# Optimization experiments

Hardware: AMD Instinct MI355X
Metric: run time of the kernel (lower is better)

The kernel has to match this reference:

```python
import jax, jax.numpy as jnp
import numpy as np

B, S, H, NH = 2, 2048, 2048, 16
HD = H // NH


def setup_inputs() -> dict:
    key = jax.random.key(0)
    ks = jax.random.split(key, 10)
    s = 1.0 / np.sqrt(H)
    x = jax.random.normal(ks[0], (B, S, H), dtype=jnp.float32)
    # additive causal mask: 0 on/below diagonal, -1e9 above
    causal = jnp.tril(jnp.ones((S, S), dtype=bool))
    mask = jnp.where(causal, 0.0, -1e9).astype(jnp.float32)[None, None]
    return {
        "x": x,
        "mask": mask,
        "wq": jax.random.normal(ks[1], (H, H), jnp.float32) * s,
        "bq": jnp.zeros((H,), jnp.float32),
        "wk": jax.random.normal(ks[2], (H, H), jnp.float32) * s,
        "bk": jnp.zeros((H,), jnp.float32),
        "wv": jax.random.normal(ks[3], (H, H), jnp.float32) * s,
        "bv": jnp.zeros((H,), jnp.float32),
        "wo": jax.random.normal(ks[4], (H, H), jnp.float32) * s,
        "bo": jnp.zeros((H,), jnp.float32),
    }


def reference(x, mask, wq, bq, wk, bk, wv, bv, wo, bo):
    b, s, _ = x.shape
    scale = HD ** (-0.5)
    # projections -> [b, nh, s, hd]
    def split_heads(t):
        return t.reshape(b, s, NH, HD).transpose(0, 2, 1, 3)
    q = split_heads(x @ wq + bq)
    k = split_heads(x @ wk + bk)
    v = split_heads(x @ wv + bv)
    scores = jnp.einsum('bhqd,bhkd->bhqk', q, k) * scale + mask
    attn = jax.nn.softmax(scores, axis=-1)
    out = jnp.einsum('bhqk,bhkd->bhqd', attn, v)
    out = out.transpose(0, 2, 1, 3).reshape(b, s, H)
    return out @ wo + bo
```

## Files before the change

### kernel.cpp

```cpp
#include <hip/hip_runtime.h>


using bf16x8 = __attribute__((ext_vector_type(8))) short;
using bf16x4 = __attribute__((ext_vector_type(4))) short;
using f32x4  = __attribute__((ext_vector_type(4))) float;

#define S_LEN 2048
#define NHEAD 16
#define HDIM  128
#define HID   2048

__device__ __forceinline__ unsigned short f2bf(float f) {
    unsigned int u = __float_as_uint(f);
    u += 0x7fffu + ((u >> 16) & 1u);
    return (unsigned short)(u >> 16);
}
__device__ __forceinline__ void gl2lds16(const void* g, void* l) {
    __builtin_amdgcn_global_load_lds(
        (const __attribute__((address_space(1))) void*)g,
        (__attribute__((address_space(3))) void*)l, 16, 0, 0);
}

__device__ __forceinline__ f32x4 pv_mfma(bf16x4 a, bf16x4 b, f32x4 c) {
#if defined(__HIP_DEVICE_COMPILE__)
#if __has_builtin(__builtin_amdgcn_mfma_f32_16x16x16bf16_1k)
    return __builtin_amdgcn_mfma_f32_16x16x16bf16_1k(a, b, c, 0, 0, 0);
#else
    asm("v_mfma_f32_16x16x16_bf16 %0, %1, %2, %0" : "+v"(c) : "v"(a), "v"(b));
    return c;
#endif
#else
    (void)a; (void)b;
    return c;
#endif
}

__global__ void convert_all(const float* __restrict__ x,
                            const float* __restrict__ w0, const float* __restrict__ w1,
                            const float* __restrict__ w2, const float* __restrict__ w3,
                            unsigned short* __restrict__ xb,
                            unsigned short* __restrict__ t0, unsigned short* __restrict__ t1,
                            unsigned short* __restrict__ t2, unsigned short* __restrict__ t3) {
    int z = blockIdx.z;
    if (z >= 4) {
        int lin = (z - 4) * 1024 + blockIdx.y * 32 + blockIdx.x;
        int i = (lin * 256 + threadIdx.x) * 4;
        float4 v = *(const float4*)(x + i);
        ushort4 o;
        o.x = f2bf(v.x); o.y = f2bf(v.y); o.z = f2bf(v.z); o.w = f2bf(v.w);
        *(ushort4*)(xb + i) = o;
        return;
    }
    __shared__ float tile[64][65];
    const float* src = (z == 0) ? w0 : (z == 1) ? w1 : (z == 2) ? w2 : w3;
    unsigned short* dst = (z == 0) ? t0 : (z == 1) ? t1 : (z == 2) ? t2 : t3;
    int r0 = blockIdx.y * 64, c0 = blockIdx.x * 64;
    int t = threadIdx.x;
    for (int i = t; i < 64 * 64; i += 256) {
        int r = i >> 6, c = i & 63;
        tile[r][c] = src[(size_t)(r0 + r) * HID + c0 + c];
    }
    __syncthreads();
    for (int i = t; i < 64 * 64; i += 256) {
        int r = i & 63, c = i >> 6;
        dst[(size_t)(c0 + c) * HID + r0 + r] = f2bf(tile[r][c]);
    }
}

__device__ __forceinline__ void sched0() { __builtin_amdgcn_sched_barrier(0); }
__device__ __forceinline__ void w_lgkm8() { asm volatile("s_waitcnt lgkmcnt(8)" ::: "memory"); sched0(); }
__device__ __forceinline__ void w_lgkm4() { asm volatile("s_waitcnt lgkmcnt(4)" ::: "memory"); sched0(); }
__device__ __forceinline__ void w_lgkm0() { asm volatile("s_waitcnt lgkmcnt(0)" ::: "memory"); sched0(); }
__device__ __forceinline__ void w_vm6() { asm volatile("s_waitcnt vmcnt(6)" ::: "memory"); sched0(); }
__device__ __forceinline__ void w_vm4() { asm volatile("s_waitcnt vmcnt(4)" ::: "memory"); sched0(); }
__device__ __forceinline__ void w_vm2() { asm volatile("s_waitcnt vmcnt(2)" ::: "memory"); sched0(); }
__device__ __forceinline__ void w_vm0() { asm volatile("s_waitcnt vmcnt(0)" ::: "memory"); sched0(); }
__device__ __forceinline__ void barx() {
    asm volatile("" ::: "memory");
    __builtin_amdgcn_s_barrier();
    asm volatile("" ::: "memory");
}

__launch_bounds__(512, 2)
__global__ void gemm8p(const unsigned short* __restrict__ A,
                       const unsigned short* __restrict__ Bt,
                       const float* __restrict__ bias0,
                       const float* __restrict__ bias1,
                       const float* __restrict__ bias2,
                       unsigned short* __restrict__ C0,
                       unsigned short* __restrict__ C1,
                       unsigned short* __restrict__ C2) {
    __shared__ __align__(16) unsigned short lds[65536];
    unsigned short* const A0 = lds;
    unsigned short* const A1 = lds + 16384;
    unsigned short* const B0 = lds + 32768;
    unsigned short* const B1 = lds + 49152;

    int vb = (blockIdx.x & 7) * 48 + (blockIdx.x >> 3);
    int m0  = (vb & 15) * 256;
    int n0g = (vb >> 4) * 256;
    int z   = n0g >> 11;
    int nb0 = n0g & 2047;

    int tid = threadIdx.x;
    int lane = tid & 63;
    int wv_ = tid >> 6;
    int wr = wv_ >> 2, wc = wv_ & 3;
    int l15 = lane & 15, quad = lane >> 4;

    int tr = tid >> 3;
    int tc = ((tid & 7) ^ (tr & 7)) << 3;
    const unsigned short* gA = A  + (size_t)(m0  + tr) * HID + tc;
    const unsigned short* gB = Bt + (size_t)(n0g + tr) * HID + tc;
    const int td8 = tid * 8;

    int arow0 = (wr * 128 + l15) * 64;
    int brow0 = (wc * 64 + l15) * 64;
    int swz[2] = { ((quad ^ (l15 & 7)) << 3), (((4 + quad) ^ (l15 & 7)) << 3) };

    f32x4 acc[8][4];
#pragma unroll
    for (int i = 0; i < 8; ++i)
#pragma unroll
        for (int j = 0; j < 4; ++j) acc[i][j] = (f32x4){0.f, 0.f, 0.f, 0.f};

    bf16x8 av[2][4];
    bf16x8 bv[2][2][2];

#define SGA(kt, half, AD) do {                                               \
    size_t _g = (size_t)((half) * 128) * HID + (size_t)(kt) * 64;            \
    gl2lds16(gA + _g,            (AD) + (half) * 8192 + td8);                \
    gl2lds16(gA + _g + 64 * HID, (AD) + (half) * 8192 + 4096 + td8); } while (0)

#define SGB(kt, half, BD) do {                                               \
    size_t _g = (size_t)((half) * 128) * HID + (size_t)(kt) * 64;            \
    gl2lds16(gB + _g,            (BD) + (half) * 8192 + td8);                \
    gl2lds16(gB + _g + 64 * HID, (BD) + (half) * 8192 + 4096 + td8); } while (0)

#define RDAV(AD, hm) do {                                                    \
    _Pragma("unroll")                                                        \
    for (int kk = 0; kk < 2; ++kk)                                           \
        _Pragma("unroll")                                                    \
        for (int mi = 0; mi < 4; ++mi)                                       \
            av[kk][mi] = *(const bf16x8*)((AD) + arow0 + (hm) * 4096         \
                                          + mi * 1024 + swz[kk]); } while (0)

#define RDBV(BD, hn) do {                                                    \
    _Pragma("unroll")                                                        \
    for (int kk = 0; kk < 2; ++kk)                                           \
        _Pragma("unroll")                                                    \
        for (int nj = 0; nj < 2; ++nj)                                       \
            bv[hn][kk][nj] = *(const bf16x8*)((BD) + brow0 + (hn) * 2048     \
                                              + nj * 1024 + swz[kk]); } while (0)

#define MFQ(hm, hn) do {                                                     \
    __builtin_amdgcn_s_setprio(1);                                           \
    _Pragma("unroll")                                                        \
    for (int kk = 0; kk < 2; ++kk)                                           \
        _Pragma("unroll")                                                    \
        for (int mi = 0; mi < 4; ++mi)                                       \
            _Pragma("unroll")                                                \
            for (int nj = 0; nj < 2; ++nj)                                   \
                acc[(hm) * 4 + mi][(hn) * 2 + nj] =                          \
                    __builtin_amdgcn_mfma_f32_16x16x32_bf16(av[kk][mi],      \
                        bv[hn][kk][nj], acc[(hm) * 4 + mi][(hn) * 2 + nj],   \
                        0, 0, 0);                                            \
    __builtin_amdgcn_s_setprio(0); sched0(); } while (0)

    SGA(0, 0, A0); SGA(0, 1, A0);
    SGB(0, 0, B0); SGB(0, 1, B0);
    SGA(1, 0, A1); SGB(1, 0, B1);
    w_vm4();
    barx();

    for (int it = 0; it < 16; ++it) {
        int t  = 2 * it;
        int t2 = (t + 2 < 32) ? t + 2 : 31;
        int t3 = (t + 3 < 32) ? t + 3 : 31;
        RDAV(A0, 0); RDBV(B0, 0);
        SGA(t + 1, 1, A1);
        w_lgkm8();
        barx(); w_lgkm0();
        MFQ(0, 0);
        barx();
        RDBV(B0, 1);
        SGB(t + 1, 1, B1);
        barx(); w_lgkm0();
        MFQ(0, 1);
        barx();
        RDAV(A0, 1);
        SGA(t2, 0, A0);
        barx(); w_lgkm0();
        MFQ(1, 0);
        barx();
        SGB(t2, 0, B0);
        barx();
        MFQ(1, 1);
        w_vm4();
        barx();
        RDAV(A1, 0); RDBV(B1, 0);
        SGA(t2, 1, A0);
        w_lgkm8();
        barx(); w_lgkm0();
        MFQ(0, 0);
        barx();
        RDBV(B1, 1);
        SGB(t2, 1, B0);
        barx(); w_lgkm0();
        MFQ(0, 1);
        barx();
        RDAV(A1, 1);
        SGA(t3, 0, A1);
        barx(); w_lgkm0();
        MFQ(1, 0);
        barx();
        SGB(t3, 0, B1);
        barx();
        MFQ(1, 1);
        w_vm4();
        barx();
    }
    asm volatile("s_waitcnt vmcnt(0) lgkmcnt(0)" ::: "memory");

#undef SGA
#undef SGB
#undef RDAV
#undef RDBV
#undef MFQ

#pragma unroll
    for (int j = 0; j < 4; ++j) {
        int n = nb0 + wc * 64 + j * 16 + l15;
        float bn = (z == 0) ? bias0[n] : (z == 1) ? bias1[n] : bias2[n];
        unsigned short* Cz = (z == 0) ? C0 : (z == 1) ? C1 : C2;
#pragma unroll
        for (int i = 0; i < 8; ++i) {
            int mb = m0 + wr * 128 + i * 16 + quad * 4;
            if (z == 2) {
                int b = mb >> 11, s = mb & 2047, h = n >> 7, d = n & 127;
                int kt = s >> 4, qv = (s >> 2) & 3, ct = d >> 4, lv = d & 15;
                size_t addr = ((((size_t)((b << 4) + h) * 128 + kt) * 4 + (ct >> 1)) * 4 + qv) * 128
                              + lv * 8 + (ct & 1) * 4;
                ushort4 o;
                o.x = f2bf(acc[i][j][0] + bn);
                o.y = f2bf(acc[i][j][1] + bn);
                o.z = f2bf(acc[i][j][2] + bn);
                o.w = f2bf(acc[i][j][3] + bn);
                *(ushort4*)&Cz[addr] = o;
            } else {
#pragma unroll
                for (int reg = 0; reg < 4; ++reg) {
                    int m = mb + reg;
                    float v = acc[i][j][reg] + bn;
                    int b = m >> 11, s = m & 2047, h = n >> 7, d = n & 127;
                    if (z == 1) {
                        int kt = s >> 4, lk = s & 15, kk = d >> 5, qk = (d >> 3) & 3, e = d & 7;
                        size_t addr = ((((size_t)((b << 4) + h) * 128 + kt) * 4 + kk) * 4 + qk) * 128
                                      + lk * 8 + e;
                        Cz[addr] = f2bf(v);
                    } else {
                        Cz[(size_t)(((b << 4) + h) * S_LEN + s) * HDIM + d] = f2bf(v);
                    }
                }
            }
        }
    }
}

__launch_bounds__(512, 2)
__global__ void gemmO(const unsigned short* __restrict__ A,
                      const unsigned short* __restrict__ Bt0,
                      const float* __restrict__ bias0,
                      float* __restrict__ Cf) {
    constexpr int NJ = 2;
    __shared__ __align__(16) unsigned short lds[2 * 16384 + 2 * NJ * 4096];
    unsigned short* const A0 = lds;
    unsigned short* const A1 = lds + 16384;
    unsigned short* const B0 = lds + 32768;
    unsigned short* const B1 = lds + 32768 + NJ * 4096;

    int vb = (blockIdx.x & 7) * 32 + (blockIdx.x >> 3);
    int m0  = (vb & 15) * 256;
    int n0g = (vb >> 4) * (NJ * 64);

    int tid = threadIdx.x;
    int lane = tid & 63;
    int wv_ = tid >> 6;
    int wr = wv_ >> 2, wc = wv_ & 3;
    int l15 = lane & 15, quad = lane >> 4;

    int tr = tid >> 3;
    int tc = ((tid & 7) ^ (tr & 7)) << 3;
    const unsigned short* gA = A   + (size_t)(m0  + tr) * HID + tc;
    const unsigned short* gB = Bt0 + (size_t)(n0g + tr) * HID + tc;
    const int td8 = tid * 8;

    int arow0 = (wr * 128 + l15) * 64;
    int brow0 = (wc * (16 * NJ) + l15) * 64;
    int sw0 = ((quad ^ (l15 & 7)) << 3);
    int sw1 = (((4 + quad) ^ (l15 & 7)) << 3);

    f32x4 acc[8][NJ];
#pragma unroll
    for (int i = 0; i < 8; ++i)
#pragma unroll
        for (int j = 0; j < NJ; ++j) acc[i][j] = (f32x4){0.f, 0.f, 0.f, 0.f};

    bf16x8 aX[4], aY[4], b0v[NJ], b1v[NJ];

#define STAGE(kt, AD, BD) do { int _kc = (kt) * 64;                          \
    gl2lds16(gA + _kc,             (AD) + td8);                              \
    gl2lds16(gA + 64 * HID + _kc,  (AD) + 4096 + td8);                       \
    gl2lds16(gA + 128 * HID + _kc, (AD) + 8192 + td8);                       \
    gl2lds16(gA + 192 * HID + _kc, (AD) + 12288 + td8);                      \
    _Pragma("unroll")                                                        \
    for (int _r = 0; _r < NJ; ++_r)                                          \
        gl2lds16(gB + (size_t)(_r * 64) * HID + _kc, (BD) + _r * 4096 + td8); } while (0)

#define LDA4(dst, AD, QB, SW) do {                                           \
    dst[0] = *(const bf16x8*)((AD) + arow0 + ((QB) + 0) * 1024 + (SW));      \
    dst[1] = *(const bf16x8*)((AD) + arow0 + ((QB) + 1) * 1024 + (SW));      \
    dst[2] = *(const bf16x8*)((AD) + arow0 + ((QB) + 2) * 1024 + (SW));      \
    dst[3] = *(const bf16x8*)((AD) + arow0 + ((QB) + 3) * 1024 + (SW)); } while (0)

#define LDB(dst, BD, SW) do {                                                \
    _Pragma("unroll")                                                        \
    for (int _n = 0; _n < NJ; ++_n)                                          \
        dst[_n] = *(const bf16x8*)((BD) + brow0 + _n * 1024 + (SW)); } while (0)

#define MF(Q, a, b) do {                                                     \
    __builtin_amdgcn_s_setprio(1);                                           \
    _Pragma("unroll")                                                        \
    for (int mi = 0; mi < 4; ++mi)                                           \
        _Pragma("unroll")                                                    \
        for (int nj = 0; nj < NJ; ++nj)                                      \
            acc[(Q) * 4 + mi][nj] =                                          \
                __builtin_amdgcn_mfma_f32_16x16x32_bf16(a[mi], b[nj],        \
                                                        acc[(Q) * 4 + mi][nj], 0, 0, 0); \
    __builtin_amdgcn_s_setprio(0); } while (0)

#define TILE(AD, BD, AN, BN_, ks) do {                                       \
    LDA4(aY, AD, 4, sw0);                                                    \
    w_lgkm4();                                                               \
    MF(0, aX, b0v);                                                          \
    LDA4(aX, AD, 0, sw1);                                                    \
    LDB(b1v, BD, sw1);                                                       \
    asm volatile("s_waitcnt lgkmcnt(6)" ::: "memory"); sched0();             \
    MF(1, aY, b0v);                                                          \
    LDA4(aY, AD, 4, sw1);                                                    \
    w_lgkm4();                                                               \
    MF(0, aX, b1v);                                                          \
    w_lgkm0();                                                               \
    barx();                                                                  \
    STAGE(ks, AD, BD);                                                       \
    w_vm6();                                                                 \
    barx();                                                                  \
    LDA4(aX, AN, 0, sw0);                                                    \
    LDB(b0v, BN_, sw0);                                                      \
    sched0();                                                                \
    MF(1, aY, b1v);                                                          \
} while (0)

    STAGE(0, A0, B0);
    STAGE(1, A1, B1);
    w_vm6();
    barx();
    LDA4(aX, A0, 0, sw0);
    LDB(b0v, B0, sw0);

    for (int t = 0; t < 32; t += 2) {
        TILE(A0, B0, A1, B1, (t + 2 < 32) ? t + 2 : 31);
        TILE(A1, B1, A0, B0, (t + 3 < 32) ? t + 3 : 31);
    }
    asm volatile("s_waitcnt vmcnt(0) lgkmcnt(0)" ::: "memory");

#undef TILE
#undef STAGE
#undef LDA4
#undef LDB
#undef MF

#pragma unroll
    for (int j = 0; j < NJ; ++j) {
        int n = n0g + wc * (16 * NJ) + j * 16 + l15;
        float bn = bias0[n];
#pragma unroll
        for (int i = 0; i < 8; ++i) {
            int mb = m0 + wr * 128 + i * 16 + quad * 4;
#pragma unroll
            for (int reg = 0; reg < 4; ++reg) {
                int m = mb + reg;
                Cf[(size_t)m * HID + n] = acc[i][j][reg] + bn;
            }
        }
    }
}

__launch_bounds__(256, 2)
__global__ void attn_kernel(const unsigned short* __restrict__ Qg,
                            const unsigned short* __restrict__ Kp,
                            const unsigned short* __restrict__ Vp,
                            unsigned short* __restrict__ O) {
    __shared__ __align__(16) unsigned short kv[2][4096];

    int linear = blockIdx.x;
    int xcd = linear & 7;
    int u = linear >> 3;
    int bh = xcd * 4 + (u & 3);
    int q = u >> 2;
    int b = bh >> 4, h = bh & 15;

    int tid = threadIdx.x, lane = tid & 63, w = tid >> 6;
    int l15 = lane & 15, quad = lane >> 4;

    const unsigned short* Qb = Qg + (size_t)bh * (S_LEN * HDIM);
    const unsigned short* Kg = Kp + (size_t)bh * 262144;
    const unsigned short* Vg = Vp + (size_t)bh * 262144;
    const float k2 = 0.08838834764831845f * 1.4426950408889634f;

    const int frag = quad * 128 + l15 * 8;
    const int td8 = tid * 8;

#define VLO(x) __builtin_shufflevector(x, x, 0, 1, 2, 3)
#define VHI(x) __builtin_shufflevector(x, x, 4, 5, 6, 7)
#define ASTAGE(kt, bf) do { size_t _g = (size_t)(kt) * 2048 + td8;             \
    gl2lds16(Kg + _g, &kv[bf][td8]);                                           \
    gl2lds16(Vg + _g, &kv[bf][2048 + td8]); } while (0)

    auto run_qblock = [&](int qb) {
        int s  = 4 * qb + w;
        int r0 = s * 16;
        int N  = 4 * qb + 4;

        bf16x8 qf[4];
#pragma unroll
        for (int kk = 0; kk < 4; ++kk)
            qf[kk] = *(const bf16x8*)&Qb[(size_t)(r0 + l15) * HDIM + kk * 32 + quad * 8];

        f32x4 o_acc[8];
#pragma unroll
        for (int c = 0; c < 8; ++c) o_acc[c] = (f32x4){0.f, 0.f, 0.f, 0.f};
        float l_part = 0.f;

        ASTAGE(0, 0);
        for (int kt = 0; kt < N; ++kt) {
            int nk = (kt + 1 < N) ? kt + 1 : kt;
            ASTAGE(nk, (kt + 1) & 1);
            w_vm2();
            barx();

            const unsigned short* KL = &kv[kt & 1][frag];
            const unsigned short* VL = &kv[kt & 1][2048 + frag];
            bf16x8 kb0 = *(const bf16x8*)(KL);
            bf16x8 kb1 = *(const bf16x8*)(KL + 512);
            bf16x8 kb2 = *(const bf16x8*)(KL + 1024);
            bf16x8 kb3 = *(const bf16x8*)(KL + 1536);
            bf16x8 v0 = *(const bf16x8*)(VL);
            bf16x8 v1 = *(const bf16x8*)(VL + 512);
            bf16x8 v2 = *(const bf16x8*)(VL + 1024);
            bf16x8 v3 = *(const bf16x8*)(VL + 1536);

            f32x4 st0 = (f32x4){0.f, 0.f, 0.f, 0.f};
            f32x4 st1 = (f32x4){0.f, 0.f, 0.f, 0.f};
            __builtin_amdgcn_s_setprio(1);
            st0 = __builtin_amdgcn_mfma_f32_16x16x32_bf16(kb0, qf[0], st0, 0, 0, 0);
            st1 = __builtin_amdgcn_mfma_f32_16x16x32_bf16(kb1, qf[1], st1, 0, 0, 0);
            st0 = __builtin_amdgcn_mfma_f32_16x16x32_bf16(kb2, qf[2], st0, 0, 0, 0);
            st1 = __builtin_amdgcn_mfma_f32_16x16x32_bf16(kb3, qf[3], st1, 0, 0, 0);
            __builtin_amdgcn_s_setprio(0);
            f32x4 stv = st0 + st1;

            float p0, p1, p2, p3;
            int doff = kt - s;
            if (doff >= 0) {
                int d16 = doff << 4;
                p0 = (d16 + quad * 4 + 0 <= l15) ? exp2f(stv[0] * k2) : 0.f;
                p1 = (d16 + quad * 4 + 1 <= l15) ? exp2f(stv[1] * k2) : 0.f;
                p2 = (d16 + quad * 4 + 2 <= l15) ? exp2f(stv[2] * k2) : 0.f;
                p3 = (d16 + quad * 4 + 3 <= l15) ? exp2f(stv[3] * k2) : 0.f;
            } else {
                p0 = exp2f(stv[0] * k2); p1 = exp2f(stv[1] * k2);
                p2 = exp2f(stv[2] * k2); p3 = exp2f(stv[3] * k2);
            }
            l_part += (p0 + p1) + (p2 + p3);

            bf16x4 pf;
            pf[0] = (short)f2bf(p0); pf[1] = (short)f2bf(p1);
            pf[2] = (short)f2bf(p2); pf[3] = (short)f2bf(p3);

            __builtin_amdgcn_s_setprio(1);
            o_acc[0] = pv_mfma(pf, VLO(v0), o_acc[0]);
            o_acc[1] = pv_mfma(pf, VHI(v0), o_acc[1]);
            o_acc[2] = pv_mfma(pf, VLO(v1), o_acc[2]);
            o_acc[3] = pv_mfma(pf, VHI(v1), o_acc[3]);
            o_acc[4] = pv_mfma(pf, VLO(v2), o_acc[4]);
            o_acc[5] = pv_mfma(pf, VHI(v2), o_acc[5]);
            o_acc[6] = pv_mfma(pf, VLO(v3), o_acc[6]);
            o_acc[7] = pv_mfma(pf, VHI(v3), o_acc[7]);
            __builtin_amdgcn_s_setprio(0);
            barx();
        }
        w_vm0();
        barx();

        float lp = l_part;
        lp += __shfl_xor(lp, 16, 64);
        lp += __shfl_xor(lp, 32, 64);
#pragma unroll
        for (int reg = 0; reg < 4; ++reg) {
            float l = __shfl(lp, quad * 4 + reg, 64);
            float inv = 1.f / l;
            int srow = r0 + quad * 4 + reg;
            unsigned short* op = O + (size_t)(b * S_LEN + srow) * HID + h * HDIM;
#pragma unroll
            for (int ct = 0; ct < 8; ++ct)
                op[ct * 16 + l15] = f2bf(o_acc[ct][reg] * inv);
        }
    };

    run_qblock(q);
    run_qblock(31 - q);

#undef ASTAGE
#undef VLO
#undef VHI
}

extern "C" void kernel_launch(void* const* d_in, const int* in_sizes, int n_in,
                              void* d_out, int out_size, void* d_ws, size_t ws_size,
                              hipStream_t stream) {
    (void)in_sizes; (void)n_in; (void)out_size; (void)ws_size;
    const float* x  = (const float*)d_in[0];
    const float* wq = (const float*)d_in[2];
    const float* bq = (const float*)d_in[3];
    const float* wk = (const float*)d_in[4];
    const float* bk = (const float*)d_in[5];
    const float* wv = (const float*)d_in[6];
    const float* bv = (const float*)d_in[7];
    const float* wo = (const float*)d_in[8];
    const float* bo = (const float*)d_in[9];
    float* out = (float*)d_out;

    unsigned short* ws = (unsigned short*)d_ws;
    const size_t WSZ = 4194304;
    unsigned short* wqT = ws;
    unsigned short* wkT = ws + WSZ;
    unsigned short* wvT = ws + 2 * WSZ;
    unsigned short* woT = ws + 3 * WSZ;
    unsigned short* xb  = ws + 4 * WSZ;
    unsigned short* Ab  = ws + 4 * WSZ;
    unsigned short* Qb  = ws + 6 * WSZ;
    unsigned short* Kb  = ws + 8 * WSZ;
    unsigned short* Vb  = ws + 10 * WSZ;

    convert_all<<<dim3(32, 32, 12), 256, 0, stream>>>(x, wq, wk, wv, wo,
                                                      xb, wqT, wkT, wvT, woT);
    gemm8p<<<dim3(384), 512, 0, stream>>>(xb, wqT, bq, bk, bv, Qb, Kb, Vb);
    attn_kernel<<<dim3(512), 256, 0, stream>>>(Qb, Kb, Vb, Ab);
    gemmO<<<dim3(256), 512, 0, stream>>>(Ab, woT, bo, out);
}
```

Baseline: 393.9 us.

## Retile QKV projection GEMM to 256x192 tiles with 512 blocks

The fused QKV projection GEMM now uses 256x192 output tiles instead of 256x256, so it launches 512 workgroups rather than 384. The aim is better balance of work across the 256 CUs (two full waves) and lower LDS use per block. Column tiles can now straddle the Q/K/V boundary, so the epilogue picks the output tensor per column. The output GEMM is turned into a template whose wait counts depend on NJ, but it still runs with the same NJ=2 configuration. The trade-off is less data reuse per tile and a reworked load/compute interleave with more barriers and waits.

```diff
diff --git a/kernel.cpp b/kernel.cpp
--- a/kernel.cpp
+++ b/kernel.cpp
@@ -68,10 +68,18 @@
 }
 
 __device__ __forceinline__ void sched0() { __builtin_amdgcn_sched_barrier(0); }
-__device__ __forceinline__ void w_lgkm8() { asm volatile("s_waitcnt lgkmcnt(8)" ::: "memory"); sched0(); }
 __device__ __forceinline__ void w_lgkm4() { asm volatile("s_waitcnt lgkmcnt(4)" ::: "memory"); sched0(); }
 __device__ __forceinline__ void w_lgkm0() { asm volatile("s_waitcnt lgkmcnt(0)" ::: "memory"); sched0(); }
-__device__ __forceinline__ void w_vm6() { asm volatile("s_waitcnt vmcnt(6)" ::: "memory"); sched0(); }
+template <int NJ> __device__ __forceinline__ void w_lgkm_4nj() {
+    if constexpr (NJ == 3) { asm volatile("s_waitcnt lgkmcnt(7)" ::: "memory"); }
+    else                   { asm volatile("s_waitcnt lgkmcnt(6)" ::: "memory"); }
+    sched0();
+}
+template <int NJ> __device__ __forceinline__ void w_vm_ns() {
+    if constexpr (NJ == 3) { asm volatile("s_waitcnt vmcnt(7)" ::: "memory"); }
+    else                   { asm volatile("s_waitcnt vmcnt(6)" ::: "memory"); }
+    sched0();
+}
 __device__ __forceinline__ void w_vm4() { asm volatile("s_waitcnt vmcnt(4)" ::: "memory"); sched0(); }
 __device__ __forceinline__ void w_vm2() { asm volatile("s_waitcnt vmcnt(2)" ::: "memory"); sched0(); }
 __device__ __forceinline__ void w_vm0() { asm volatile("s_waitcnt vmcnt(0)" ::: "memory"); sched0(); }
@@ -82,7 +90,7 @@
 }
 
 __launch_bounds__(512, 2)
-__global__ void gemm8p(const unsigned short* __restrict__ A,
+__global__ void gemm8q(const unsigned short* __restrict__ A,
                        const unsigned short* __restrict__ Bt,
                        const float* __restrict__ bias0,
                        const float* __restrict__ bias1,
@@ -90,17 +98,15 @@
                        unsigned short* __restrict__ C0,
                        unsigned short* __restrict__ C1,
                        unsigned short* __restrict__ C2) {
-    __shared__ __align__(16) unsigned short lds[65536];
+    __shared__ __align__(16) unsigned short lds[57344];
     unsigned short* const A0 = lds;
     unsigned short* const A1 = lds + 16384;
     unsigned short* const B0 = lds + 32768;
-    unsigned short* const B1 = lds + 49152;
-
-    int vb = (blockIdx.x & 7) * 48 + (blockIdx.x >> 3);
+    unsigned short* const B1 = lds + 45056;
+
+    int vb = (blockIdx.x & 7) * 64 + (blockIdx.x >> 3);
     int m0  = (vb & 15) * 256;
-    int n0g = (vb >> 4) * 256;
-    int z   = n0g >> 11;
-    int nb0 = n0g & 2047;
+    int n0g = (vb >> 4) * 192;
 
     int tid = threadIdx.x;
     int lane = tid & 63;
@@ -114,62 +120,53 @@
     const unsigned short* gB = Bt + (size_t)(n0g + tr) * HID + tc;
     const int td8 = tid * 8;
 
-    int arow0 = (wr * 128 + l15) * 64;
-    int brow0 = (wc * 64 + l15) * 64;
+    int arow0 = (wr * 64 + l15) * 64;
+    int brow0 = (wc * 48 + l15) * 64;
     int swz[2] = { ((quad ^ (l15 & 7)) << 3), (((4 + quad) ^ (l15 & 7)) << 3) };
 
-    f32x4 acc[8][4];
+    f32x4 acc[8][3];
 #pragma unroll
     for (int i = 0; i < 8; ++i)
 #pragma unroll
-        for (int j = 0; j < 4; ++j) acc[i][j] = (f32x4){0.f, 0.f, 0.f, 0.f};
-
-    bf16x8 av[2][4];
-    bf16x8 bv[2][2][2];
+        for (int j = 0; j < 3; ++j) acc[i][j] = (f32x4){0.f, 0.f, 0.f, 0.f};
+
+    bf16x8 av[4];
+    bf16x8 bv[2][3];
 
 #define SGA(kt, half, AD) do {                                               \
     size_t _g = (size_t)((half) * 128) * HID + (size_t)(kt) * 64;            \
     gl2lds16(gA + _g,            (AD) + (half) * 8192 + td8);                \
     gl2lds16(gA + _g + 64 * HID, (AD) + (half) * 8192 + 4096 + td8); } while (0)
 
-#define SGB(kt, half, BD) do {                                               \
-    size_t _g = (size_t)((half) * 128) * HID + (size_t)(kt) * 64;            \
-    gl2lds16(gB + _g,            (BD) + (half) * 8192 + td8);                \
-    gl2lds16(gB + _g + 64 * HID, (BD) + (half) * 8192 + 4096 + td8); } while (0)
-
-#define RDAV(AD, hm) do {                                                    \
+#define SGB3(kt, third, BD) do {                                             \
+    size_t _g = (size_t)((third) * 64) * HID + (size_t)(kt) * 64;            \
+    gl2lds16(gB + _g, (BD) + (third) * 4096 + td8); } while (0)
+
+#define RDA(AD, hm, kk) do {                                                 \
     _Pragma("unroll")                                                        \
-    for (int kk = 0; kk < 2; ++kk)                                           \
-        _Pragma("unroll")                                                    \
-        for (int mi = 0; mi < 4; ++mi)                                       \
-            av[kk][mi] = *(const bf16x8*)((AD) + arow0 + (hm) * 4096         \
-                                          + mi * 1024 + swz[kk]); } while (0)
-
-#define RDBV(BD, hn) do {                                                    \
+    for (int mi = 0; mi < 4; ++mi)                                           \
+        av[mi] = *(const bf16x8*)((AD) + arow0 + (hm) * 8192                 \
+                                  + mi * 1024 + swz[kk]); } while (0)
+
+#define RDB(BD, kk) do {                                                     \
     _Pragma("unroll")                                                        \
-    for (int kk = 0; kk < 2; ++kk)                                           \
-        _Pragma("unroll")                                                    \
-        for (int nj = 0; nj < 2; ++nj)                                       \
-            bv[hn][kk][nj] = *(const bf16x8*)((BD) + brow0 + (hn) * 2048     \
-                                              + nj * 1024 + swz[kk]); } while (0)
-
-#define MFQ(hm, hn) do {                                                     \
+    for (int nj = 0; nj < 3; ++nj)                                           \
+        bv[kk][nj] = *(const bf16x8*)((BD) + brow0 + nj * 1024 + swz[kk]); } while (0)
+
+#define MFQ(hm, kk) do {                                                     \
     __builtin_amdgcn_s_setprio(1);                                           \
     _Pragma("unroll")                                                        \
-    for (int kk = 0; kk < 2; ++kk)                                           \
+    for (int mi = 0; mi < 4; ++mi)                                           \
         _Pragma("unroll")                                                    \
-        for (int mi = 0; mi < 4; ++mi)                                       \
-            _Pragma("unroll")                                                \
-            for (int nj = 0; nj < 2; ++nj)                                   \
-                acc[(hm) * 4 + mi][(hn) * 2 + nj] =                          \
-                    __builtin_amdgcn_mfma_f32_16x16x32_bf16(av[kk][mi],      \
-                        bv[hn][kk][nj], acc[(hm) * 4 + mi][(hn) * 2 + nj],   \
-                        0, 0, 0);                                            \
+        for (int nj = 0; nj < 3; ++nj)                                       \
+            acc[(hm) * 4 + mi][nj] =                                         \
+                __builtin_amdgcn_mfma_f32_16x16x32_bf16(av[mi], bv[kk][nj],  \
+                    acc[(hm) * 4 + mi][nj], 0, 0, 0);                        \
     __builtin_amdgcn_s_setprio(0); sched0(); } while (0)
 
     SGA(0, 0, A0); SGA(0, 1, A0);
-    SGB(0, 0, B0); SGB(0, 1, B0);
-    SGA(1, 0, A1); SGB(1, 0, B1);
+    SGB3(0, 0, B0); SGB3(0, 1, B0); SGB3(0, 2, B0);
+    SGA(1, 0, A1); SGB3(1, 0, B1); SGB3(1, 1, B1);
     w_vm4();
     barx();
 
@@ -177,45 +174,43 @@
         int t  = 2 * it;
         int t2 = (t + 2 < 32) ? t + 2 : 31;
         int t3 = (t + 3 < 32) ? t + 3 : 31;
-        RDAV(A0, 0); RDBV(B0, 0);
-        SGA(t + 1, 1, A1);
-        w_lgkm8();
+        RDA(A0, 0, 0); RDB(B0, 0);
+        SGA(t + 1, 1, A1); SGB3(t + 1, 2, B1);
         barx(); w_lgkm0();
         MFQ(0, 0);
         barx();
-        RDBV(B0, 1);
-        SGB(t + 1, 1, B1);
+        RDA(A0, 0, 1); RDB(B0, 1);
         barx(); w_lgkm0();
         MFQ(0, 1);
         barx();
-        RDAV(A0, 1);
+        RDA(A0, 1, 0);
         SGA(t2, 0, A0);
         barx(); w_lgkm0();
         MFQ(1, 0);
         barx();
-        SGB(t2, 0, B0);
-        barx();
+        RDA(A0, 1, 1);
+        SGB3(t2, 0, B0); SGB3(t2, 1, B0);
+        barx(); w_lgkm0();
         MFQ(1, 1);
         w_vm4();
         barx();
-        RDAV(A1, 0); RDBV(B1, 0);
-        SGA(t2, 1, A0);
-        w_lgkm8();
+        RDA(A1, 0, 0); RDB(B1, 0);
+        SGA(t2, 1, A0); SGB3(t2, 2, B0);
         barx(); w_lgkm0();
         MFQ(0, 0);
         barx();
-        RDBV(B1, 1);
-        SGB(t2, 1, B0);
+        RDA(A1, 0, 1); RDB(B1, 1);
         barx(); w_lgkm0();
         MFQ(0, 1);
         barx();
-        RDAV(A1, 1);
+        RDA(A1, 1, 0);
         SGA(t3, 0, A1);
         barx(); w_lgkm0();
         MFQ(1, 0);
         barx();
-        SGB(t3, 0, B1);
-        barx();
+        RDA(A1, 1, 1);
+        SGB3(t3, 0, B1); SGB3(t3, 1, B1);
+        barx(); w_lgkm0();
         MFQ(1, 1);
         w_vm4();
         barx();
@@ -223,21 +218,23 @@
     asm volatile("s_waitcnt vmcnt(0) lgkmcnt(0)" ::: "memory");
 
 #undef SGA
-#undef SGB
-#undef RDAV
-#undef RDBV
+#undef SGB3
+#undef RDA
+#undef RDB
 #undef MFQ
 
 #pragma unroll
-    for (int j = 0; j < 4; ++j) {
-        int n = nb0 + wc * 64 + j * 16 + l15;
-        float bn = (z == 0) ? bias0[n] : (z == 1) ? bias1[n] : bias2[n];
-        unsigned short* Cz = (z == 0) ? C0 : (z == 1) ? C1 : C2;
+    for (int j = 0; j < 3; ++j) {
+        int n = n0g + wc * 48 + j * 16 + l15;
+        int zj = n >> 11;
+        int nn = n & 2047;
+        float bn = (zj == 0) ? bias0[nn] : (zj == 1) ? bias1[nn] : bias2[nn];
+        unsigned short* Cz = (zj == 0) ? C0 : (zj == 1) ? C1 : C2;
 #pragma unroll
         for (int i = 0; i < 8; ++i) {
-            int mb = m0 + wr * 128 + i * 16 + quad * 4;
-            if (z == 2) {
-                int b = mb >> 11, s = mb & 2047, h = n >> 7, d = n & 127;
+            int mb = m0 + (i >> 2) * 128 + wr * 64 + (i & 3) * 16 + quad * 4;
+            if (zj == 2) {
+                int b = mb >> 11, s = mb & 2047, h = nn >> 7, d = nn & 127;
                 int kt = s >> 4, qv = (s >> 2) & 3, ct = d >> 4, lv = d & 15;
                 size_t addr = ((((size_t)((b << 4) + h) * 128 + kt) * 4 + (ct >> 1)) * 4 + qv) * 128
                               + lv * 8 + (ct & 1) * 4;
@@ -252,8 +249,8 @@
                 for (int reg = 0; reg < 4; ++reg) {
                     int m = mb + reg;
                     float v = acc[i][j][reg] + bn;
-                    int b = m >> 11, s = m & 2047, h = n >> 7, d = n & 127;
-                    if (z == 1) {
+                    int b = m >> 11, s = m & 2047, h = nn >> 7, d = nn & 127;
+                    if (zj == 1) {
                         int kt = s >> 4, lk = s & 15, kk = d >> 5, qk = (d >> 3) & 3, e = d & 7;
                         size_t addr = ((((size_t)((b << 4) + h) * 128 + kt) * 4 + kk) * 4 + qk) * 128
                                       + lk * 8 + e;
@@ -267,12 +264,12 @@
     }
 }
 
+template <int MODE, int NJ>
 __launch_bounds__(512, 2)
-__global__ void gemmO(const unsigned short* __restrict__ A,
+__global__ void gemmT(const unsigned short* __restrict__ A,
                       const unsigned short* __restrict__ Bt0,
                       const float* __restrict__ bias0,
                       float* __restrict__ Cf) {
-    constexpr int NJ = 2;
     __shared__ __align__(16) unsigned short lds[2 * 16384 + 2 * NJ * 4096];
     unsigned short* const A0 = lds;
     unsigned short* const A1 = lds + 16384;
@@ -345,7 +342,7 @@
     MF(0, aX, b0v);                                                          \
     LDA4(aX, AD, 0, sw1);                                                    \
     LDB(b1v, BD, sw1);                                                       \
-    asm volatile("s_waitcnt lgkmcnt(6)" ::: "memory"); sched0();             \
+    w_lgkm_4nj<NJ>();                                                        \
     MF(1, aY, b0v);                                                          \
     LDA4(aY, AD, 4, sw1);                                                    \
     w_lgkm4();                                                               \
@@ -353,7 +350,7 @@
     w_lgkm0();                                                               \
     barx();                                                                  \
     STAGE(ks, AD, BD);                                                       \
-    w_vm6();                                                                 \
+    w_vm_ns<NJ>();                                                           \
     barx();                                                                  \
     LDA4(aX, AN, 0, sw0);                                                    \
     LDB(b0v, BN_, sw0);                                                      \
@@ -363,7 +360,7 @@
 
     STAGE(0, A0, B0);
     STAGE(1, A1, B1);
-    w_vm6();
+    w_vm_ns<NJ>();
     barx();
     LDA4(aX, A0, 0, sw0);
     LDB(b0v, B0, sw0);
@@ -555,7 +552,7 @@
 
     convert_all<<<dim3(32, 32, 12), 256, 0, stream>>>(x, wq, wk, wv, wo,
                                                       xb, wqT, wkT, wvT, woT);
-    gemm8p<<<dim3(384), 512, 0, stream>>>(xb, wqT, bq, bk, bv, Qb, Kb, Vb);
+    gemm8q<<<dim3(512), 512, 0, stream>>>(xb, wqT, bq, bk, bv, Qb, Kb, Vb);
     attn_kernel<<<dim3(512), 256, 0, stream>>>(Qb, Kb, Vb, Ab);
-    gemmO<<<dim3(256), 512, 0, stream>>>(Ab, woT, bo, out);
-}
+    gemmT<0, 2><<<dim3(256), 512, 0, stream>>>(Ab, woT, bo, out);
+}
```

Result: faster. 376.1 us (median of 2 runs) (-4.5%).
